# Kernel tuning notes

Measured on AMD Instinct MI355X. Metric: run time of the kernel, lower is better.

The kernel has to match this reference:

```python
import jax, jax.numpy as jnp
import numpy as np

B, T, D = 2, 1024, 1024
H, HKV = 16, 8
HD = D // H           # 64
NREP = H // HKV       # 2
NLAYERS = 3
MAXKV = T * NLAYERS   # 3072
EPS = 1e-5


def setup_inputs() -> dict:
    key = jax.random.key(0)
    ks = jax.random.split(key, 8)
    # rotary tables over full accumulated-KV range
    inv_freq = 1.0 / (10000.0 ** (jnp.arange(0, HD, 2, dtype=jnp.float32) / HD))  # (HD/2,)
    t = jnp.arange(MAXKV, dtype=jnp.float32)
    freqs = jnp.outer(t, inv_freq)  # (MAXKV, HD/2)
    return {
        "x": jax.random.normal(ks[0], (B, T, D), jnp.float32),
        "cos": jnp.cos(freqs),
        "sin": jnp.sin(freqs),
        "q_w": jax.random.normal(ks[1], (NLAYERS, D, D), jnp.float32) * 0.02,
        "k_w": jax.random.normal(ks[2], (NLAYERS, D // NREP, D), jnp.float32) * 0.02,
        "v_w": jax.random.normal(ks[3], (NLAYERS, D // NREP, D), jnp.float32) * 0.02,
        "ln_w": jnp.ones((NLAYERS, D), jnp.float32),
        "lam": jax.random.normal(ks[4], (NLAYERS,), jnp.float32) * 0.1,
        "out_w": jax.random.normal(ks[5], (D, D), jnp.float32) * 0.02,
        "final_ln_w": jnp.ones((D,), jnp.float32),
        "alpha": jnp.ones((1,), jnp.float32),
    }


def rmsnorm(x, w):
    return x * jax.lax.rsqrt(jnp.mean(x * x, axis=-1, keepdims=True) + EPS) * w


def rope(x, cos, sin):
    # x: (B, L, h, HD); cos/sin: (MAXKV, HD/2); flash_attn non-interleaved rotary
    L = x.shape[1]
    c = jnp.concatenate([cos[:L], cos[:L]], axis=-1)[None, :, None, :]
    s = jnp.concatenate([sin[:L], sin[:L]], axis=-1)[None, :, None, :]
    x1, x2 = jnp.split(x, 2, axis=-1)
    rot = jnp.concatenate([-x2, x1], axis=-1)
    return x * c + rot * s


def reference(x, cos, sin, q_w, k_w, v_w, ln_w, lam, out_w, final_ln_w, alpha):
    scale = HD ** -0.5
    # lambda weights: layernorm over sigmoid of the 3 scalars (biased var, eps=1e-5)
    s = jax.nn.sigmoid(lam)
    lw = (s - s.mean()) * jax.lax.rsqrt(s.var() + EPS)
    qidx = jnp.arange(T)
    k_list, v_list = [], []
    acc = jnp.zeros_like(x)
    for i in range(NLAYERS):
        q = (x @ q_w[i].T).reshape(B, T, H, HD)
        k = (x @ k_w[i].T).reshape(B, T, HKV, HD)
        v = (x @ v_w[i].T).reshape(B, T, HKV, HD)
        k_list.append(k)
        v_list.append(v)
        K = jnp.concatenate(k_list, axis=1)  # (B, L, HKV, HD), L=(i+1)*T
        V = jnp.concatenate(v_list, axis=1)
        L = K.shape[1]
        qr = rope(q, cos, sin)
        Kr = rope(K, cos, sin)  # whole buffer re-rotated each layer, as in original
        Kr = jnp.repeat(Kr, NREP, axis=2)  # GQA expand
        Vr = jnp.repeat(V, NREP, axis=2)
        scores = jnp.einsum('bqhd,bkhd->bhqk', qr, Kr) * scale
        # flash_attn causal=True with kv_len > q_len aligns bottom-right
        mask = jnp.arange(L)[None, :] <= (qidx + (L - T))[:, None]
        scores = jnp.where(mask[None, None], scores, -jnp.inf)
        attn = jax.nn.softmax(scores, axis=-1)
        o = jnp.einsum('bhqk,bkhd->bqhd', attn, Vr).reshape(B, T, D)
        acc = acc + rmsnorm(o, ln_w[i]) * lw[i]
    out = rmsnorm(acc + alpha * x, final_ln_w)
    return out @ out_w.T
```

## Files before the change

### kernel.cpp

```cpp
#include <hip/hip_runtime.h>
#include <type_traits>
#include <utility>

typedef unsigned short u16;
typedef unsigned int u32;
typedef short short8 __attribute__((ext_vector_type(8)));
typedef __bf16 bf16x8 __attribute__((ext_vector_type(8)));
typedef float floatx4 __attribute__((ext_vector_type(4)));

template <typename V, typename = void> struct MfmaTakes : std::false_type {};
template <typename V>
struct MfmaTakes<V, std::void_t<decltype(__builtin_amdgcn_mfma_f32_16x16x32_bf16(
    std::declval<V>(), std::declval<V>(), std::declval<floatx4>(), 0, 0, 0))>>
    : std::true_type {};

template <typename V>
__device__ __forceinline__ floatx4 mfma_impl(V a, V b, floatx4 c, std::true_type) {
  return __builtin_amdgcn_mfma_f32_16x16x32_bf16(a, b, c, 0, 0, 0);
}
template <typename V>
__device__ __forceinline__ floatx4 mfma_impl(V a, V b, floatx4 c, std::false_type) {
  return __builtin_amdgcn_mfma_f32_16x16x32_bf16(
      __builtin_bit_cast(bf16x8, a), __builtin_bit_cast(bf16x8, b), c, 0, 0, 0);
}
__device__ __forceinline__ floatx4 MFMA16(short8 a, short8 b, floatx4 c) {
  return mfma_impl<short8>(a, b, c, MfmaTakes<short8>{});
}

__device__ __forceinline__ u16 f2bf(float f) {
  union { float f; unsigned u; } x; x.f = f;
  unsigned r = (x.u + 0x7fffu + ((x.u >> 16) & 1u)) >> 16;
  return (u16)r;
}
__device__ __forceinline__ float bf2f(u16 v) {
  union { unsigned u; float f; } x; x.u = ((unsigned)v) << 16; return x.f;
}
__device__ __forceinline__ u32 packbf(float lo, float hi) {
  return (__float_as_uint(hi) & 0xffff0000u) | (__float_as_uint(lo) >> 16);
}

#if defined(__has_builtin)
#if __has_builtin(__builtin_amdgcn_global_load_lds)
#define HAS_GLLDS 1
#endif
#endif
__device__ __forceinline__ void stage16(const u16* g, u16* lbase, int lane) {
#ifdef HAS_GLLDS
  __builtin_amdgcn_global_load_lds(
      (__attribute__((address_space(1))) void*)(g),
      (__attribute__((address_space(3))) void*)(lbase), 16, 0, 0);
#else
  *(uint4*)(lbase + lane * 8) = *(const uint4*)g;
#endif
}

__global__ __launch_bounds__(256) void prep_kernel(
    const float* __restrict__ x, const float* __restrict__ qw,
    const float* __restrict__ kw, const float* __restrict__ vw,
    const float* __restrict__ outw, const float* __restrict__ lam,
    u16* __restrict__ xb, u16* __restrict__ wcat, u16* __restrict__ outwb,
    float* __restrict__ lwbuf) {
  size_t gid = (size_t)blockIdx.x * 256 + threadIdx.x;
  if (gid == 0) {
    float s0 = 1.f / (1.f + expf(-lam[0]));
    float s1 = 1.f / (1.f + expf(-lam[1]));
    float s2 = 1.f / (1.f + expf(-lam[2]));
    float mean = (s0 + s1 + s2) * (1.f / 3.f);
    float d0 = s0 - mean, d1 = s1 - mean, d2 = s2 - mean;
    float var = (d0 * d0 + d1 * d1 + d2 * d2) * (1.f / 3.f);
    float r = rsqrtf(var + 1e-5f);
    lwbuf[0] = d0 * r; lwbuf[1] = d1 * r; lwbuf[2] = d2 * r;
  }
  if (gid < 524288) {
    float4 v = ((const float4*)x)[gid];
    ushort4 o; o.x = f2bf(v.x); o.y = f2bf(v.y); o.z = f2bf(v.z); o.w = f2bf(v.w);
    ((ushort4*)xb)[gid] = o;
    return;
  }
  size_t g2 = gid - 524288;
  if (g2 < 1572864) {
    int col4 = (int)(g2 & 255);
    int n = (int)(g2 >> 8);
    int layer = n >> 11, r = n & 2047;
    const float* srcrow;
    if (r < 1024) srcrow = qw + ((size_t)(layer * 1024 + r) << 10);
    else if (r < 1536) srcrow = kw + ((size_t)(layer * 512 + (r - 1024)) << 10);
    else srcrow = vw + ((size_t)(layer * 512 + (r - 1536)) << 10);
    float4 v = ((const float4*)srcrow)[col4];
    ushort4 o; o.x = f2bf(v.x); o.y = f2bf(v.y); o.z = f2bf(v.z); o.w = f2bf(v.w);
    ((ushort4*)wcat)[g2] = o;
    return;
  }
  size_t g3 = g2 - 1572864;
  if (g3 < 262144) {
    float4 v = ((const float4*)outw)[g3];
    ushort4 o; o.x = f2bf(v.x); o.y = f2bf(v.y); o.z = f2bf(v.z); o.w = f2bf(v.w);
    ((ushort4*)outwb)[g3] = o;
  }
}

__global__ __launch_bounds__(256) void gemm128(
    const u16* __restrict__ A, const u16* __restrict__ Bw,
    void* __restrict__ Cp, int N, int K, int obf16) {
  __shared__ u16 As[128][64];
  __shared__ u16 Bs[128][64];
  const unsigned flat = blockIdx.x;
  const int bm = (flat >> 3) & 15;
  const int bn = ((flat >> 7) << 3) + (flat & 7);
  const int tid = threadIdx.x;
  const int wave = tid >> 6, lane = tid & 63;
  const int quad = lane >> 4, l16 = lane & 15;
  const int wm = wave & 1, wn = wave >> 1;
  const int srow = lane >> 3, skc = (lane & 7) * 8;
  floatx4 acc[4][4];
#pragma unroll
  for (int i = 0; i < 4; i++)
#pragma unroll
    for (int j = 0; j < 4; j++) { acc[i][j][0] = 0.f; acc[i][j][1] = 0.f; acc[i][j][2] = 0.f; acc[i][j][3] = 0.f; }
  const u16* Abase = A + (size_t)(bm * 128) * K;
  const u16* Bbase = Bw + (size_t)(bn * 128) * K;
  for (int k0 = 0; k0 < K; k0 += 64) {
    __syncthreads();
#pragma unroll
    for (int i = 0; i < 4; i++) {
      int ch = wave * 4 + i;
      stage16(Abase + (size_t)(ch * 8 + srow) * K + k0 + skc, &As[ch * 8][0], lane);
      stage16(Bbase + (size_t)(ch * 8 + srow) * K + k0 + skc, &Bs[ch * 8][0], lane);
    }
    __syncthreads();
#pragma unroll
    for (int kf = 0; kf < 2; kf++) {
      short8 af[4], bf[4];
#pragma unroll
      for (int mi = 0; mi < 4; mi++)
        af[mi] = *(const short8*)(&As[wm * 64 + mi * 16 + l16][kf * 32 + quad * 8]);
#pragma unroll
      for (int ni = 0; ni < 4; ni++)
        bf[ni] = *(const short8*)(&Bs[wn * 64 + ni * 16 + l16][kf * 32 + quad * 8]);
#pragma unroll
      for (int mi = 0; mi < 4; mi++)
#pragma unroll
        for (int ni = 0; ni < 4; ni++)
          acc[mi][ni] = MFMA16(af[mi], bf[ni], acc[mi][ni]);
    }
  }
  float* Cf = (float*)Cp;
  u16* Cb = (u16*)Cp;
#pragma unroll
  for (int mi = 0; mi < 4; mi++)
#pragma unroll
    for (int ni = 0; ni < 4; ni++)
#pragma unroll
      for (int r = 0; r < 4; r++) {
        int row = bm * 128 + wm * 64 + mi * 16 + quad * 4 + r;
        int col = bn * 128 + wn * 64 + ni * 16 + l16;
        if (obf16) Cb[(size_t)row * N + col] = f2bf(acc[mi][ni][r]);
        else Cf[(size_t)row * N + col] = acc[mi][ni][r];
      }
}

__global__ __launch_bounds__(256) void gemm_bt(
    const u16* __restrict__ A, const u16* __restrict__ Bw,
    float* __restrict__ C, int N, int K) {
  __shared__ u16 As[64][72];
  __shared__ u16 Bs[64][72];
  const int bm = blockIdx.x, bn = blockIdx.y;
  const int tid = threadIdx.x;
  const int wave = tid >> 6, lane = tid & 63;
  const int quad = lane >> 4, l16 = lane & 15;
  const int lr = tid >> 2, lc = (tid & 3) << 4;
  floatx4 acc[4];
#pragma unroll
  for (int i = 0; i < 4; i++) { acc[i][0] = 0.f; acc[i][1] = 0.f; acc[i][2] = 0.f; acc[i][3] = 0.f; }
  const u16* Arow = A + (size_t)(bm * 64 + lr) * K;
  const u16* Brow = Bw + (size_t)(bn * 64 + lr) * K;
  for (int k0 = 0; k0 < K; k0 += 64) {
    __syncthreads();
    *(uint4*)(&As[lr][lc])     = *(const uint4*)(Arow + k0 + lc);
    *(uint4*)(&As[lr][lc + 8]) = *(const uint4*)(Arow + k0 + lc + 8);
    *(uint4*)(&Bs[lr][lc])     = *(const uint4*)(Brow + k0 + lc);
    *(uint4*)(&Bs[lr][lc + 8]) = *(const uint4*)(Brow + k0 + lc + 8);
    __syncthreads();
    const int mrow = wave * 16 + l16;
    short8 a0 = *(const short8*)(&As[mrow][quad * 8]);
    short8 a1 = *(const short8*)(&As[mrow][32 + quad * 8]);
#pragma unroll
    for (int ns = 0; ns < 4; ns++) {
      short8 b0 = *(const short8*)(&Bs[ns * 16 + l16][quad * 8]);
      short8 b1 = *(const short8*)(&Bs[ns * 16 + l16][32 + quad * 8]);
      acc[ns] = MFMA16(a0, b0, acc[ns]);
      acc[ns] = MFMA16(a1, b1, acc[ns]);
    }
  }
#pragma unroll
  for (int ns = 0; ns < 4; ns++)
#pragma unroll
    for (int r = 0; r < 4; r++) {
      int row = bm * 64 + wave * 16 + quad * 4 + r;
      int col = bn * 64 + ns * 16 + l16;
      C[(size_t)row * N + col] = acc[ns][r];
    }
}

__global__ __launch_bounds__(256) void reshape_kernel(
    const u16* __restrict__ qkvb, const float* __restrict__ cosb,
    const float* __restrict__ sinb, u16* __restrict__ qr,
    u16* __restrict__ kr, u16* __restrict__ vtg) {
  __shared__ u16 T[64][72];
  const int bid = blockIdx.x, tid = threadIdx.x;
  union U8 { uint4 v; u16 s[8]; };
  union F8 { float4 v[2]; float f[8]; };
  if (bid < 2304) {
    unsigned gid = (unsigned)bid * 256 + tid;
    if (gid < 393216u) {
      int d8 = gid & 3, t = (gid >> 2) & 1023, h = (gid >> 12) & 15;
      int b = (gid >> 16) & 1, layer = gid >> 17;
      size_t src = (size_t)(b * 1024 + t) * 6144 + layer * 2048 + h * 64 + d8 * 8;
      U8 xa, xc; xa.v = *(const uint4*)(qkvb + src); xc.v = *(const uint4*)(qkvb + src + 32);
      F8 C, S;
      const float4* cp = (const float4*)(cosb + (size_t)t * 32 + d8 * 8);
      const float4* sp = (const float4*)(sinb + (size_t)t * 32 + d8 * 8);
      C.v[0] = cp[0]; C.v[1] = cp[1]; S.v[0] = sp[0]; S.v[1] = sp[1];
      U8 o1, o2;
#pragma unroll
      for (int j = 0; j < 8; j++) {
        float x1 = bf2f(xa.s[j]), x2 = bf2f(xc.s[j]);
        o1.s[j] = f2bf((x1 * C.f[j] - x2 * S.f[j]) * 0.125f);
        o2.s[j] = f2bf((x2 * C.f[j] + x1 * S.f[j]) * 0.125f);
      }
      size_t dst = ((((size_t)layer * 2 + b) * 16 + h) * 1024 + t) * 64 + d8 * 8;
      *(uint4*)(qr + dst) = o1.v;
      *(uint4*)(qr + dst + 32) = o2.v;
      return;
    }
    unsigned g2 = gid - 393216u;
    if (g2 < 196608u) {
      int d8 = g2 & 3, t = (g2 >> 2) & 1023, h = (g2 >> 12) & 7;
      int b = (g2 >> 15) & 1, layer = g2 >> 16;
      int pos = layer * 1024 + t;
      size_t src = (size_t)(b * 1024 + t) * 6144 + layer * 2048 + 1024 + h * 64 + d8 * 8;
      U8 xa, xc; xa.v = *(const uint4*)(qkvb + src); xc.v = *(const uint4*)(qkvb + src + 32);
      F8 C, S;
      const float4* cp = (const float4*)(cosb + (size_t)pos * 32 + d8 * 8);
      const float4* sp = (const float4*)(sinb + (size_t)pos * 32 + d8 * 8);
      C.v[0] = cp[0]; C.v[1] = cp[1]; S.v[0] = sp[0]; S.v[1] = sp[1];
      U8 o1, o2;
#pragma unroll
      for (int j = 0; j < 8; j++) {
        float x1 = bf2f(xa.s[j]), x2 = bf2f(xc.s[j]);
        o1.s[j] = f2bf(x1 * C.f[j] - x2 * S.f[j]);
        o2.s[j] = f2bf(x2 * C.f[j] + x1 * S.f[j]);
      }
      size_t dst = (((size_t)b * 8 + h) * 3072 + pos) * 64 + d8 * 8;
      *(uint4*)(kr + dst) = o1.v;
      *(uint4*)(kr + dst + 32) = o2.v;
    }
    return;
  }
  const int b2 = bid - 2304;
  const int xt = b2 & 15;
  const int y = b2 >> 4;
  const int layer = y >> 4, b = (y >> 3) & 1, h = y & 7;
  const int t0 = xt * 64;
  {
    const int p = tid >> 2, dc = (tid & 3) * 16;
    const u16* src = qkvb + (size_t)(b * 1024 + t0 + p) * 6144 + layer * 2048 + 1536 + h * 64 + dc;
    U8 u0, u1;
    u0.v = *(const uint4*)(src);
    u1.v = *(const uint4*)(src + 8);
#pragma unroll
    for (int j = 0; j < 8; j++) { T[dc + j][p] = u0.s[j]; T[dc + 8 + j][p] = u1.s[j]; }
  }
  __syncthreads();
  {
    const int d = tid >> 2, pc = (tid & 3) * 16;
    u16* dst = vtg + ((size_t)((b * 8 + h) * 64 + d)) * 3072 + layer * 1024 + t0 + pc;
    *(uint4*)(dst) = *(const uint4*)(&T[d][pc]);
    *(uint4*)(dst + 8) = *(const uint4*)(&T[d][pc + 8]);
  }
}

__global__ __launch_bounds__(256) void attn_v4(
    const u16* __restrict__ qr, const u16* __restrict__ kr,
    const u16* __restrict__ vt, float* __restrict__ obS,
    float* __restrict__ lbufp) {
  __shared__ u16 Kt[64][70];
  __shared__ u16 Vt[64][70];
  __shared__ u16 Pw[4][2][16][70];
  const unsigned flat = blockIdx.x;
  const int bhz = (int)((flat >> 6) * 8 + (flat & 7));
  const int qtile = 7 - (int)((flat >> 3) & 7);
  const int z = bhz >> 5;
  const int bh = bhz & 31;
  const int lay = (0x012221u >> (z * 4)) & 0xF;
  const int c   = (0x012100u >> (z * 4)) & 0xF;
  const int b = bh >> 4, h = bh & 15, hk = h >> 1;
  const int tid = threadIdx.x, wave = tid >> 6, lane = tid & 63;
  const int quad = lane >> 4, l16 = lane & 15;
  const int kt0 = c * 16;
  const int kt1 = (c == lay) ? (lay * 16 + 2 * qtile + 2) : (kt0 + 16);
  const int maskkt = lay * 16 + 2 * qtile;
  const int qeffbase = lay * 1024 + qtile * 128 + wave * 32;
  const u16* qpb = qr + ((((size_t)lay * 2 + b) * 16 + h) * 1024
                         + qtile * 128 + wave * 32 + l16) * 64 + quad * 8;
  short8 qf[2][2];
  qf[0][0] = *(const short8*)(qpb);
  qf[0][1] = *(const short8*)(qpb + 32);
  qf[1][0] = *(const short8*)(qpb + 1024);
  qf[1][1] = *(const short8*)(qpb + 1056);
  const short8 ones = {16256, 16256, 16256, 16256, 16256, 16256, 16256, 16256};
  floatx4 oacc[2][4];
#pragma unroll
  for (int nt = 0; nt < 2; nt++)
#pragma unroll
    for (int dt = 0; dt < 4; dt++) { oacc[nt][dt][0] = 0.f; oacc[nt][dt][1] = 0.f; oacc[nt][dt][2] = 0.f; oacc[nt][dt][3] = 0.f; }
  floatx4 lacc[2];
  lacc[0][0] = 0.f; lacc[0][1] = 0.f; lacc[0][2] = 0.f; lacc[0][3] = 0.f;
  lacc[1] = lacc[0];
  const int sr = tid >> 2, sc = (tid & 3) << 4;
  const u16* kp = kr + ((size_t)(b * 8 + hk) * 3072 + kt0 * 64 + sr) * 64 + sc;
  const u16* vp = vt + ((size_t)(b * 8 + hk) * 64 + sr) * 3072 + kt0 * 64 + sc;
  uint4 kA = *(const uint4*)(kp), kB = *(const uint4*)(kp + 8);
  uint4 vA = *(const uint4*)(vp), vB = *(const uint4*)(vp + 8);
  for (int kt = kt0; kt < kt1; kt++) {
    kp += 4096; vp += 64;
    __syncthreads();
    *(uint4*)(&Kt[sr][sc])     = kA;
    *(uint4*)(&Kt[sr][sc + 8]) = kB;
    *(uint4*)(&Vt[sr][sc])     = vA;
    *(uint4*)(&Vt[sr][sc + 8]) = vB;
    if (kt + 1 < kt1) {
      kA = *(const uint4*)(kp); kB = *(const uint4*)(kp + 8);
      vA = *(const uint4*)(vp); vB = *(const uint4*)(vp + 8);
    }
    __syncthreads();
    const bool needmask = (kt >= maskkt);
#pragma unroll
    for (int mt = 0; mt < 4; mt++) {
      short8 kfa = *(const short8*)(&Kt[mt * 16 + l16][quad * 8]);
      short8 kfb = *(const short8*)(&Kt[mt * 16 + l16][32 + quad * 8]);
      const int keyb = kt * 64 + mt * 16 + quad * 4;
#pragma unroll
      for (int nt = 0; nt < 2; nt++) {
        floatx4 s; s[0] = 0.f; s[1] = 0.f; s[2] = 0.f; s[3] = 0.f;
        s = MFMA16(kfa, qf[nt][0], s);
        s = MFMA16(kfb, qf[nt][1], s);
        float p0 = __expf(s[0]), p1 = __expf(s[1]);
        float p2 = __expf(s[2]), p3 = __expf(s[3]);
        if (needmask) {
          int qpos = qeffbase + nt * 16 + l16;
          if (keyb + 0 > qpos) p0 = 0.f;
          if (keyb + 1 > qpos) p1 = 0.f;
          if (keyb + 2 > qpos) p2 = 0.f;
          if (keyb + 3 > qpos) p3 = 0.f;
        }
        uint2 st; st.x = packbf(p0, p1); st.y = packbf(p2, p3);
        *(uint2*)(&Pw[wave][nt][l16][mt * 16 + quad * 4]) = st;
      }
    }
#pragma unroll
    for (int kc = 0; kc < 2; kc++) {
      short8 pf0 = *(const short8*)(&Pw[wave][0][l16][kc * 32 + quad * 8]);
      short8 pf1 = *(const short8*)(&Pw[wave][1][l16][kc * 32 + quad * 8]);
      lacc[0] = MFMA16(ones, pf0, lacc[0]);
      lacc[1] = MFMA16(ones, pf1, lacc[1]);
#pragma unroll
      for (int dt = 0; dt < 4; dt++) {
        short8 vf = *(const short8*)(&Vt[dt * 16 + l16][kc * 32 + quad * 8]);
        oacc[0][dt] = MFMA16(vf, pf0, oacc[0][dt]);
        oacc[1][dt] = MFMA16(vf, pf1, oacc[1][dt]);
      }
    }
  }
  float* Pf = (float*)(&Pw[wave][0][0][0]);
  const int tt = lane >> 2, dd = (lane & 3) << 2;
#pragma unroll
  for (int nt = 0; nt < 2; nt++) {
    int t = qtile * 128 + wave * 32 + nt * 16 + l16;
    if (quad == 0)
      lbufp[((size_t)z * 2048 + b * 1024 + t) * 16 + h] = lacc[nt][0];
    int t2 = qtile * 128 + wave * 32 + nt * 16 + tt;
    float* orow = obS + ((size_t)(z * 2 + b) * 1024 + t2) * 1024 + h * 64 + dd;
#pragma unroll
    for (int dt = 0; dt < 4; dt++) {
      *(floatx4*)(&Pf[nt * 320 + l16 * 20 + quad * 4]) = oacc[nt][dt];
      floatx4 val = *(const floatx4*)(&Pf[nt * 320 + tt * 20 + dd]);
      *(floatx4*)(orow + dt * 16) = val;
    }
  }
}

__device__ __forceinline__ float block_sum(float v, float* red) {
  v += __shfl_xor(v, 32); v += __shfl_xor(v, 16); v += __shfl_xor(v, 8);
  v += __shfl_xor(v, 4);  v += __shfl_xor(v, 2);  v += __shfl_xor(v, 1);
  __syncthreads();
  if ((threadIdx.x & 63) == 0) red[threadIdx.x >> 6] = v;
  __syncthreads();
  return red[0] + red[1] + red[2] + red[3];
}

__global__ __launch_bounds__(256) void fused_norm(
    const float* __restrict__ obS, const float* __restrict__ lbufp,
    const float* __restrict__ x, const float* __restrict__ lnw,
    const float* __restrict__ lwbuf, const float* __restrict__ flnw,
    const float* __restrict__ alphap, u16* __restrict__ y) {
  __shared__ float red[4];
  const int row = blockIdx.x, tid = threadIdx.x;
  float a[4] = {0.f, 0.f, 0.f, 0.f};
  const int nsl[3] = {1, 2, 3};
  const int sl[3][3] = {{5, 0, 0}, {0, 4, 0}, {1, 2, 3}};
#pragma unroll
  for (int l = 0; l < 3; l++) {
    float o0 = 0.f, o1 = 0.f, o2 = 0.f, o3 = 0.f, ls = 0.f;
#pragma unroll
    for (int si = 0; si < 3; si++) {
      if (si >= nsl[l]) break;
      int z = sl[l][si];
      float4 v = ((const float4*)(obS + ((size_t)z * 2048 + row) * 1024))[tid];
      o0 += v.x; o1 += v.y; o2 += v.z; o3 += v.w;
      ls += lbufp[((size_t)z * 2048 + row) * 16 + (tid >> 4)];
    }
    float linv = 1.f / ls;
    float v0 = o0 * linv, v1 = o1 * linv, v2 = o2 * linv, v3 = o3 * linv;
    float ss = v0 * v0 + v1 * v1 + v2 * v2 + v3 * v3;
    ss = block_sum(ss, red);
    float rstd = rsqrtf(ss * (1.f / 1024.f) + 1e-5f);
    float lw = lwbuf[l];
    float4 w = ((const float4*)(lnw + (size_t)l * 1024))[tid];
    a[0] += v0 * rstd * w.x * lw;
    a[1] += v1 * rstd * w.y * lw;
    a[2] += v2 * rstd * w.z * lw;
    a[3] += v3 * rstd * w.w * lw;
  }
  const float aa = alphap[0];
  float4 xv = ((const float4*)(x + (size_t)row * 1024))[tid];
  float v0 = a[0] + aa * xv.x, v1 = a[1] + aa * xv.y;
  float v2 = a[2] + aa * xv.z, v3 = a[3] + aa * xv.w;
  float ss = v0 * v0 + v1 * v1 + v2 * v2 + v3 * v3;
  ss = block_sum(ss, red);
  float rstd = rsqrtf(ss * (1.f / 1024.f) + 1e-5f);
  float4 fw = ((const float4*)flnw)[tid];
  ushort4 o;
  o.x = f2bf(v0 * rstd * fw.x); o.y = f2bf(v1 * rstd * fw.y);
  o.z = f2bf(v2 * rstd * fw.z); o.w = f2bf(v3 * rstd * fw.w);
  ((ushort4*)(y + (size_t)row * 1024))[tid] = o;
}

extern "C" void kernel_launch(void* const* d_in, const int* in_sizes, int n_in,
                              void* d_out, int out_size, void* d_ws, size_t ws_size,
                              hipStream_t stream) {
  const float* x     = (const float*)d_in[0];
  const float* cosb  = (const float*)d_in[1];
  const float* sinb  = (const float*)d_in[2];
  const float* qw    = (const float*)d_in[3];
  const float* kw    = (const float*)d_in[4];
  const float* vw    = (const float*)d_in[5];
  const float* lnw   = (const float*)d_in[6];
  const float* lam   = (const float*)d_in[7];
  const float* outw  = (const float*)d_in[8];
  const float* flnw  = (const float*)d_in[9];
  const float* alphap= (const float*)d_in[10];
  float* out = (float*)d_out;
  char* ws = (char*)d_ws;
  u16*   xb    = (u16*)  (ws + 0);
  u16*   wcat  = (u16*)  (ws + 4194304);
  u16*   qkvb  = (u16*)  (ws + 16777216);
  float* obS   = (float*)(ws + 0);
  u16*   outwb = (u16*)  (ws + 50331648);
  float* lwbuf = (float*)(ws + 52428800);
  u16*   qr    = (u16*)  (ws + 52429824);
  u16*   kr    = (u16*)  (ws + 65012736);
  u16*   vt    = (u16*)  (ws + 71304192);
  float* lbufp = (float*)(ws + 77595648);
  u16*   yb    = (u16*)  (ws + 78382080);

  prep_kernel<<<9216, 256, 0, stream>>>(x, qw, kw, vw, outw, lam, xb, wcat, outwb, lwbuf);
  gemm128<<<768, 256, 0, stream>>>(xb, wcat, qkvb, 6144, 1024, 1);
  reshape_kernel<<<3072, 256, 0, stream>>>(qkvb, cosb, sinb, qr, kr, vt);
  attn_v4<<<1536, 256, 0, stream>>>(qr, kr, vt, obS, lbufp);
  fused_norm<<<2048, 256, 0, stream>>>(obS, lbufp, x, lnw, lwbuf, flnw, alphap, yb);
  gemm_bt<<<dim3(32, 16), 256, 0, stream>>>(yb, outwb, out, 1024, 1024);
}
```

Measured before the change: 285.4 us.

## Halve attention KV tile and rebalance causal splits across z-slices

The attention kernel now processes 32-key tiles instead of 64. The KV range of each (layer, q-tile) is split evenly across the z-slices that serve that layer (1, 2 or 3 splits), replacing the fixed 16-tile chunks, so causal work is balanced per block. The P staging buffer shrinks and V fragments are hoisted per tile, which cuts LDS use and may raise occupancy. The cost is twice as many loop iterations and barriers per key, and smaller MFMA batches between syncs.

```diff
diff --git a/kernel.cpp b/kernel.cpp
--- a/kernel.cpp
+++ b/kernel.cpp
@@ -280,26 +280,32 @@
   }
 }
 
-__global__ __launch_bounds__(256) void attn_v4(
+__global__ __launch_bounds__(256) void attn_v5(
     const u16* __restrict__ qr, const u16* __restrict__ kr,
     const u16* __restrict__ vt, float* __restrict__ obS,
     float* __restrict__ lbufp) {
-  __shared__ u16 Kt[64][70];
-  __shared__ u16 Vt[64][70];
-  __shared__ u16 Pw[4][2][16][70];
+  __shared__ u16 Kt[32][72];
+  __shared__ u16 Vtt[64][40];
+  __shared__ u16 Pw[4][16][40];
   const unsigned flat = blockIdx.x;
   const int bhz = (int)((flat >> 6) * 8 + (flat & 7));
   const int qtile = 7 - (int)((flat >> 3) & 7);
   const int z = bhz >> 5;
   const int bh = bhz & 31;
-  const int lay = (0x012221u >> (z * 4)) & 0xF;
-  const int c   = (0x012100u >> (z * 4)) & 0xF;
+  const int lay = (z == 5) ? 0 : ((z == 0 || z == 4) ? 1 : 2);
+  const int n = lay * 32 + qtile * 4 + 4;
+  int kt0, kt1;
+  if (lay == 0) { kt0 = 0; kt1 = n; }
+  else if (lay == 1) { int hf = n >> 1; kt0 = (z == 0) ? 0 : hf; kt1 = (z == 0) ? hf : n; }
+  else {
+    int t1 = n / 3, t2 = (2 * n) / 3;
+    kt0 = (z == 1) ? 0 : ((z == 2) ? t1 : t2);
+    kt1 = (z == 1) ? t1 : ((z == 2) ? t2 : n);
+  }
+  const int maskkt = lay * 32 + qtile * 4;
   const int b = bh >> 4, h = bh & 15, hk = h >> 1;
   const int tid = threadIdx.x, wave = tid >> 6, lane = tid & 63;
   const int quad = lane >> 4, l16 = lane & 15;
-  const int kt0 = c * 16;
-  const int kt1 = (c == lay) ? (lay * 16 + 2 * qtile + 2) : (kt0 + 16);
-  const int maskkt = lay * 16 + 2 * qtile;
   const int qeffbase = lay * 1024 + qtile * 128 + wave * 32;
   const u16* qpb = qr + ((((size_t)lay * 2 + b) * 16 + h) * 1024
                          + qtile * 128 + wave * 32 + l16) * 64 + quad * 8;
@@ -317,29 +323,26 @@
   floatx4 lacc[2];
   lacc[0][0] = 0.f; lacc[0][1] = 0.f; lacc[0][2] = 0.f; lacc[0][3] = 0.f;
   lacc[1] = lacc[0];
-  const int sr = tid >> 2, sc = (tid & 3) << 4;
-  const u16* kp = kr + ((size_t)(b * 8 + hk) * 3072 + kt0 * 64 + sr) * 64 + sc;
-  const u16* vp = vt + ((size_t)(b * 8 + hk) * 64 + sr) * 3072 + kt0 * 64 + sc;
-  uint4 kA = *(const uint4*)(kp), kB = *(const uint4*)(kp + 8);
-  uint4 vA = *(const uint4*)(vp), vB = *(const uint4*)(vp + 8);
+  const int ksr = tid >> 3, ksc = (tid & 7) * 8;
+  const int vdr = tid >> 2, vdc = (tid & 3) * 8;
+  const u16* kp = kr + ((size_t)(b * 8 + hk) * 3072 + kt0 * 32 + ksr) * 64 + ksc;
+  const u16* vp = vt + ((size_t)(b * 8 + hk) * 64 + vdr) * 3072 + kt0 * 32 + vdc;
+  uint4 kA = *(const uint4*)kp;
+  uint4 vA = *(const uint4*)vp;
   for (int kt = kt0; kt < kt1; kt++) {
-    kp += 4096; vp += 64;
-    __syncthreads();
-    *(uint4*)(&Kt[sr][sc])     = kA;
-    *(uint4*)(&Kt[sr][sc + 8]) = kB;
-    *(uint4*)(&Vt[sr][sc])     = vA;
-    *(uint4*)(&Vt[sr][sc + 8]) = vB;
-    if (kt + 1 < kt1) {
-      kA = *(const uint4*)(kp); kB = *(const uint4*)(kp + 8);
-      vA = *(const uint4*)(vp); vB = *(const uint4*)(vp + 8);
-    }
+    kp += 2048; vp += 32;
+    __syncthreads();
+    *(uint4*)(&Kt[ksr][ksc])  = kA;
+    *(uint4*)(&Vtt[vdr][vdc]) = vA;
+    if (kt + 1 < kt1) { kA = *(const uint4*)kp; vA = *(const uint4*)vp; }
     __syncthreads();
     const bool needmask = (kt >= maskkt);
-#pragma unroll
-    for (int mt = 0; mt < 4; mt++) {
+    uint2 pk[2][2];
+#pragma unroll
+    for (int mt = 0; mt < 2; mt++) {
       short8 kfa = *(const short8*)(&Kt[mt * 16 + l16][quad * 8]);
       short8 kfb = *(const short8*)(&Kt[mt * 16 + l16][32 + quad * 8]);
-      const int keyb = kt * 64 + mt * 16 + quad * 4;
+      const int keyb = kt * 32 + mt * 16 + quad * 4;
 #pragma unroll
       for (int nt = 0; nt < 2; nt++) {
         floatx4 s; s[0] = 0.f; s[1] = 0.f; s[2] = 0.f; s[3] = 0.f;
@@ -354,25 +357,26 @@
           if (keyb + 2 > qpos) p2 = 0.f;
           if (keyb + 3 > qpos) p3 = 0.f;
         }
-        uint2 st; st.x = packbf(p0, p1); st.y = packbf(p2, p3);
-        *(uint2*)(&Pw[wave][nt][l16][mt * 16 + quad * 4]) = st;
+        pk[mt][nt].x = packbf(p0, p1);
+        pk[mt][nt].y = packbf(p2, p3);
       }
     }
-#pragma unroll
-    for (int kc = 0; kc < 2; kc++) {
-      short8 pf0 = *(const short8*)(&Pw[wave][0][l16][kc * 32 + quad * 8]);
-      short8 pf1 = *(const short8*)(&Pw[wave][1][l16][kc * 32 + quad * 8]);
-      lacc[0] = MFMA16(ones, pf0, lacc[0]);
-      lacc[1] = MFMA16(ones, pf1, lacc[1]);
-#pragma unroll
-      for (int dt = 0; dt < 4; dt++) {
-        short8 vf = *(const short8*)(&Vt[dt * 16 + l16][kc * 32 + quad * 8]);
-        oacc[0][dt] = MFMA16(vf, pf0, oacc[0][dt]);
-        oacc[1][dt] = MFMA16(vf, pf1, oacc[1][dt]);
-      }
-    }
-  }
-  float* Pf = (float*)(&Pw[wave][0][0][0]);
+    short8 vf[4];
+#pragma unroll
+    for (int dt = 0; dt < 4; dt++)
+      vf[dt] = *(const short8*)(&Vtt[dt * 16 + l16][quad * 8]);
+#pragma unroll
+    for (int nt = 0; nt < 2; nt++) {
+      *(uint2*)(&Pw[wave][l16][quad * 4])      = pk[0][nt];
+      *(uint2*)(&Pw[wave][l16][16 + quad * 4]) = pk[1][nt];
+      short8 pf = *(const short8*)(&Pw[wave][l16][quad * 8]);
+      lacc[nt] = MFMA16(ones, pf, lacc[nt]);
+#pragma unroll
+      for (int dt = 0; dt < 4; dt++)
+        oacc[nt][dt] = MFMA16(vf[dt], pf, oacc[nt][dt]);
+    }
+  }
+  float* Pf = (float*)(&Pw[wave][0][0]);
   const int tt = lane >> 2, dd = (lane & 3) << 2;
 #pragma unroll
   for (int nt = 0; nt < 2; nt++) {
@@ -383,8 +387,8 @@
     float* orow = obS + ((size_t)(z * 2 + b) * 1024 + t2) * 1024 + h * 64 + dd;
 #pragma unroll
     for (int dt = 0; dt < 4; dt++) {
-      *(floatx4*)(&Pf[nt * 320 + l16 * 20 + quad * 4]) = oacc[nt][dt];
-      floatx4 val = *(const floatx4*)(&Pf[nt * 320 + tt * 20 + dd]);
+      *(floatx4*)(&Pf[l16 * 20 + quad * 4]) = oacc[nt][dt];
+      floatx4 val = *(const floatx4*)(&Pf[tt * 20 + dd]);
       *(floatx4*)(orow + dt * 16) = val;
     }
   }
@@ -477,7 +481,7 @@
   prep_kernel<<<9216, 256, 0, stream>>>(x, qw, kw, vw, outw, lam, xb, wcat, outwb, lwbuf);
   gemm128<<<768, 256, 0, stream>>>(xb, wcat, qkvb, 6144, 1024, 1);
   reshape_kernel<<<3072, 256, 0, stream>>>(qkvb, cosb, sinb, qr, kr, vt);
-  attn_v4<<<1536, 256, 0, stream>>>(qr, kr, vt, obS, lbufp);
+  attn_v5<<<1536, 256, 0, stream>>>(qr, kr, vt, obS, lbufp);
   fused_norm<<<2048, 256, 0, stream>>>(obS, lbufp, x, lnw, lwbuf, flnw, alphap, yb);
   gemm_bt<<<dim3(32, 16), 256, 0, stream>>>(yb, outwb, out, 1024, 1024);
 }
```

Result: faster. 262.5 us (-8.0%).
